# Kernel optimization log

Measured on AMD Instinct MI355X. Metric: run time of the kernel, lower is better.

The kernel has to match this reference:

```python
import jax, jax.numpy as jnp
import numpy as np
from jax import lax

B, T, L = 256, 512, 128


def setup_inputs() -> dict:
    key = jax.random.key(0)
    k1, k2, k3 = jax.random.split(key, 3)
    labels = jax.random.randint(k1, (B, T), 0, L)
    y_true = jax.nn.one_hot(labels, L, dtype=jnp.float32)  # [B,T,L]
    y_pred = jax.random.normal(k2, (B, T, L), dtype=jnp.float32)
    trans = jax.random.normal(k3, (L, L), dtype=jnp.float32) * 0.1
    return {"y_true": y_true, "y_pred": y_pred, "trans": trans}


def reference(y_true, y_pred, trans):
    # ---- log partition via forward algorithm (lax.scan over time) ----
    init = y_pred[:, 0]  # [B,L] initial alpha

    def step(alpha, emit):  # alpha [B,L], emit [B,L]
        # alpha[:, i, None] + trans[i, j] -> logsumexp over previous label i
        new = jax.nn.logsumexp(alpha[:, :, None] + trans[None, :, :], axis=1) + emit
        return new, None

    emits = jnp.swapaxes(y_pred[:, 1:], 0, 1)  # [T-1,B,L]
    final_alpha, _ = lax.scan(step, init, emits)  # [B,L]
    log_norm = jax.nn.logsumexp(final_alpha, axis=1, keepdims=True)  # [B,1]

    # ---- path score (unnormalized log prob of the true path) ----
    point_score = jnp.sum(y_pred * y_true, axis=(1, 2), keepdims=False)[:, None]  # [B,1]
    trans_score = jnp.einsum('bti,btj,ij->b', y_true[:, :-1], y_true[:, 1:], trans)[:, None]  # [B,1]

    return log_norm - (point_score + trans_score)  # [B,1]
```

## Files before the change

### kernel.cpp

```cpp
#include <hip/hip_runtime.h>

typedef float    f32x4  __attribute__((ext_vector_type(4)));
typedef short    s16x8  __attribute__((ext_vector_type(8)));
typedef unsigned uivec2 __attribute__((ext_vector_type(2)));
typedef unsigned uivec4 __attribute__((ext_vector_type(4)));

#define Tt 512
#define Ll 128
#define CH 32
#define CL 16
#define NR 31
#define NRECB 248
#define NSCORE 256

#define WS_PT 0
#define WS_TR 256
#define WS_KR 512
#define WS_KB (512 + 256*NR)
#define WS_RV (512 + 2*256*NR)
#define WS_BV (WS_RV + 256*NR*128)

__device__ __forceinline__ ushort bf16rn(float f) {
  unsigned u = __float_as_uint(f);
  u += 0x7FFFu + ((u >> 16) & 1u);
  return (ushort)(u >> 16);
}
__device__ __forceinline__ unsigned cvtpk(float a, float b) {
  unsigned d;
  asm("v_cvt_pk_bf16_f32 %0, %1, %2" : "=v"(d) : "v"(a), "v"(b));
  return d;
}
__device__ __forceinline__ float4 expf4(float4 v) {
  float4 r; r.x = __expf(v.x); r.y = __expf(v.y); r.z = __expf(v.z); r.w = __expf(v.w);
  return r;
}
__device__ __forceinline__ float4 mul4(float4 v, float s) {
  v.x *= s; v.y *= s; v.z *= s; v.w *= s; return v;
}

__global__ __attribute__((amdgpu_flat_work_group_size(256, 256),
                          amdgpu_waves_per_eu(1)))
void crf_main(const float* __restrict__ yt_g, const float* __restrict__ yp_g,
              const float* __restrict__ tr_g, float* __restrict__ wsf)
{
  __shared__ __align__(16) char smem[32768];
  const int tid = threadIdx.x, wv = tid >> 6, l = tid & 63;
  const int bid = blockIdx.x;

  bool isrec; int sidx = 0, ridx = 0;
  if (bid < 2 * NRECB) { isrec = (bid & 1); sidx = ridx = bid >> 1; }
  else { isrec = false; sidx = NRECB + (bid - 2 * NRECB); }

  if (!isrec) {
    int*   lab_s = (int*)smem;
    float* redp  = (float*)(smem + 2048);
    float* redt  = (float*)(smem + 2080);
    const int b = sidx;
    const float4* yp4 = (const float4*)(yp_g + (size_t)b * Tt * Ll);
    const float4* yt4 = (const float4*)(yt_g + (size_t)b * Tt * Ll);
    float pt = 0.f;
    #pragma unroll 4
    for (int i = 0; i < 64; ++i) {
      int f = tid + i * 256;
      float4 a = yp4[f], y = yt4[f];
      pt += a.x * y.x + a.y * y.y + a.z * y.z + a.w * y.w;
      int t = f >> 5, jb = (f & 31) << 2;
      if (y.x > .5f) lab_s[t] = jb;
      if (y.y > .5f) lab_s[t] = jb + 1;
      if (y.z > .5f) lab_s[t] = jb + 2;
      if (y.w > .5f) lab_s[t] = jb + 3;
    }
    __syncthreads();
    float trl = 0.f;
    for (int t0 = tid; t0 < Tt - 1; t0 += 256)
      trl += tr_g[lab_s[t0] * Ll + lab_s[t0 + 1]];
    #pragma unroll
    for (int o = 32; o; o >>= 1) { pt += __shfl_xor(pt, o); trl += __shfl_xor(trl, o); }
    if (l == 0) { redp[wv] = pt; redt[wv] = trl; }
    __syncthreads();
    if (tid == 0) {
      wsf[WS_PT + b] = redp[0] + redp[1] + redp[2] + redp[3];
      wsf[WS_TR + b] = redt[0] + redt[1] + redt[2] + redt[3];
    }
    return;
  }

  const int task = ridx * 4 + wv;
  const bool FWD = task < 496;
  int g, c;
  if (FWD) { g = task / 31; c = task % 31; }
  else     { int t2 = task - 496; g = t2 / 31; c = t2 % 31 + 1; }
  const int b0  = g * 16;
  const int l15 = l & 15, q = l >> 4;
  const int t_hi = (c == CH - 1) ? (Tt - 1) : (c * CL + CL);
  const int t_lo = c * CL + 1;
  const int n    = FWD ? CL : (t_hi - t_lo + 1);

  s16x8 Bf[8][4];
  if (FWD) {
    #pragma unroll
    for (int kt = 0; kt < 4; ++kt)
      #pragma unroll
      for (int e = 0; e < 8; ++e) {
        const int jin = 32 * kt + 16 * (e >> 2) + 4 * q + (e & 3);
        const float* rp_ = tr_g + jin * Ll + l15;
        #pragma unroll
        for (int tl = 0; tl < 8; ++tl)
          Bf[tl][kt][e] = (short)bf16rn(__expf(rp_[16 * tl]));
      }
  } else {
    #pragma unroll
    for (int tl = 0; tl < 8; ++tl) {
      const float* rp_ = tr_g + (l15 + 16 * tl) * Ll + 4 * q;
      #pragma unroll
      for (int kt = 0; kt < 4; ++kt)
        #pragma unroll
        for (int r = 0; r < 2; ++r) {
          float4 tv = *(const float4*)(rp_ + 32 * kt + 16 * r);
          Bf[tl][kt][4 * r + 0] = (short)bf16rn(__expf(tv.x));
          Bf[tl][kt][4 * r + 1] = (short)bf16rn(__expf(tv.y));
          Bf[tl][kt][4 * r + 2] = (short)bf16rn(__expf(tv.z));
          Bf[tl][kt][4 * r + 3] = (short)bf16rn(__expf(tv.w));
        }
    }
  }

  const unsigned sbase = (unsigned)(size_t)(&smem[0]);
  const unsigned wvoff = (unsigned)(wv * 8192);
  const unsigned lane8 = (unsigned)(l * 8);
  const int wroff = wv * 8192 + l15 * 32 + q * 8;
  const float* emb = yp_g + (size_t)(b0 + l15) * (Tt * Ll) + 4 * q;
  float Kacc = 0.f;

#define LOADSLOT(S, TAU)                                                      \
  { const float* ep_ = emb + (size_t)(TAU) * Ll;                              \
    S##0 = *(const float4*)(ep_ + 0);   S##1 = *(const float4*)(ep_ + 16);    \
    S##2 = *(const float4*)(ep_ + 32);  S##3 = *(const float4*)(ep_ + 48);    \
    S##4 = *(const float4*)(ep_ + 64);  S##5 = *(const float4*)(ep_ + 80);    \
    S##6 = *(const float4*)(ep_ + 96);  S##7 = *(const float4*)(ep_ + 112); }

#define TRREAD8(RBUF, T0,T1,T2,T3,T4,T5,T6,T7)                                \
  { unsigned ra_ = sbase + wvoff + (unsigned)((RBUF) * 4096) + lane8;         \
    asm volatile(                                                             \
      "ds_read_b64_tr_b16 %0, %8 offset:0\n\t"                                \
      "ds_read_b64_tr_b16 %1, %8 offset:512\n\t"                              \
      "ds_read_b64_tr_b16 %2, %8 offset:1024\n\t"                             \
      "ds_read_b64_tr_b16 %3, %8 offset:1536\n\t"                             \
      "ds_read_b64_tr_b16 %4, %8 offset:2048\n\t"                             \
      "ds_read_b64_tr_b16 %5, %8 offset:2560\n\t"                             \
      "ds_read_b64_tr_b16 %6, %8 offset:3072\n\t"                             \
      "ds_read_b64_tr_b16 %7, %8 offset:3584\n\t"                             \
      "s_waitcnt lgkmcnt(0)"                                                  \
      : "=v"(T0), "=v"(T1), "=v"(T2), "=v"(T3),                               \
        "=v"(T4), "=v"(T5), "=v"(T6), "=v"(T7)                                \
      : "v"(ra_) : "memory"); }

#define BUILDA(A_, TA, TB, WA, WB_)                                           \
  { uivec4 au_;                                                               \
    au_.x = cvtpk(__uint_as_float(TA.x << 16) * WA.x,                         \
                  __uint_as_float(TA.x & 0xFFFF0000u) * WA.y);                \
    au_.y = cvtpk(__uint_as_float(TA.y << 16) * WA.z,                         \
                  __uint_as_float(TA.y & 0xFFFF0000u) * WA.w);                \
    au_.z = cvtpk(__uint_as_float(TB.x << 16) * WB_.x,                        \
                  __uint_as_float(TB.x & 0xFFFF0000u) * WB_.y);               \
    au_.w = cvtpk(__uint_as_float(TB.y << 16) * WB_.z,                        \
                  __uint_as_float(TB.y & 0xFFFF0000u) * WB_.w);               \
    A_ = __builtin_bit_cast(s16x8, au_); }

#define MFMAW(WBUF)                                                           \
  { f32x4 dd[8];                                                              \
    _Pragma("unroll")                                                         \
    for (int tl = 0; tl < 8; ++tl) {                                          \
      f32x4 z = {0.f, 0.f, 0.f, 0.f};                                         \
      z = __builtin_amdgcn_mfma_f32_16x16x32_bf16(A0, Bf[tl][0], z, 0, 0, 0); \
      z = __builtin_amdgcn_mfma_f32_16x16x32_bf16(A1, Bf[tl][1], z, 0, 0, 0); \
      z = __builtin_amdgcn_mfma_f32_16x16x32_bf16(A2, Bf[tl][2], z, 0, 0, 0); \
      z = __builtin_amdgcn_mfma_f32_16x16x32_bf16(A3, Bf[tl][3], z, 0, 0, 0); \
      dd[tl] = z;                                                             \
    }                                                                         \
    _Pragma("unroll")                                                         \
    for (int tl = 0; tl < 8; ++tl) {                                          \
      uivec2 w_;                                                              \
      w_.x = cvtpk(dd[tl][0], dd[tl][1]);                                     \
      w_.y = cvtpk(dd[tl][2], dd[tl][3]);                                     \
      *(uivec2*)(smem + wroff + (WBUF) * 4096 + tl * 512) = w_;               \
    } }

#define MULT(RBUF, WBUF, S, REN, PT, PSLOT)                                   \
  { asm volatile("s_waitcnt lgkmcnt(0)" ::: "memory");                        \
    uivec2 t0, t1, t2, t3, t4, t5, t6, t7;                                    \
    TRREAD8(RBUF, t0, t1, t2, t3, t4, t5, t6, t7)                             \
    float4 we0 = expf4(S##0), we1 = expf4(S##1), we2 = expf4(S##2),           \
           we3 = expf4(S##3), we4 = expf4(S##4), we5 = expf4(S##5),           \
           we6 = expf4(S##6), we7 = expf4(S##7);                              \
    if (REN) {                                                                \
      float pf = __uint_as_float(__builtin_amdgcn_readfirstlane(t0.x << 16)); \
      Kacc += __logf(pf);                                                     \
      float rs = __builtin_amdgcn_rcpf(pf);                                   \
      we0 = mul4(we0, rs); we1 = mul4(we1, rs); we2 = mul4(we2, rs);          \
      we3 = mul4(we3, rs); we4 = mul4(we4, rs); we5 = mul4(we5, rs);          \
      we6 = mul4(we6, rs); we7 = mul4(we7, rs);                               \
    }                                                                         \
    s16x8 A0, A1, A2, A3;                                                     \
    BUILDA(A0, t0, t1, we0, we1)                                              \
    BUILDA(A1, t2, t3, we2, we3)                                              \
    BUILDA(A2, t4, t5, we4, we5)                                              \
    BUILDA(A3, t6, t7, we6, we7)                                              \
    MFMAW(WBUF)                                                               \
    if ((PT) >= 0) LOADSLOT(PSLOT, PT) }

  float4 SA0, SA1, SA2, SA3, SA4, SA5, SA6, SA7;
  float4 SB0, SB1, SB2, SB3, SB4, SB5, SB6, SB7;
  const int tau1 = FWD ? (t_lo - 1) : t_hi;
  const int tau2 = FWD ? t_lo : (t_hi - 1);
  LOADSLOT(SB, tau1)
  LOADSLOT(SA, tau2)

  {
    s16x8 A0, A1, A2, A3;
    if (FWD && c > 0) {
      uivec4 au; au.x = au.y = au.z = au.w = 0x3F803F80u;
      A0 = __builtin_bit_cast(s16x8, au); A1 = A0; A2 = A0; A3 = A0;
    } else {
      float4 we0 = expf4(SB0), we1 = expf4(SB1), we2 = expf4(SB2),
             we3 = expf4(SB3), we4 = expf4(SB4), we5 = expf4(SB5),
             we6 = expf4(SB6), we7 = expf4(SB7);
      uivec4 a0; a0.x = cvtpk(we0.x, we0.y); a0.y = cvtpk(we0.z, we0.w);
      a0.z = cvtpk(we1.x, we1.y); a0.w = cvtpk(we1.z, we1.w);
      uivec4 a1; a1.x = cvtpk(we2.x, we2.y); a1.y = cvtpk(we2.z, we2.w);
      a1.z = cvtpk(we3.x, we3.y); a1.w = cvtpk(we3.z, we3.w);
      uivec4 a2; a2.x = cvtpk(we4.x, we4.y); a2.y = cvtpk(we4.z, we4.w);
      a2.z = cvtpk(we5.x, we5.y); a2.w = cvtpk(we5.z, we5.w);
      uivec4 a3; a3.x = cvtpk(we6.x, we6.y); a3.y = cvtpk(we6.z, we6.w);
      a3.z = cvtpk(we7.x, we7.y); a3.w = cvtpk(we7.z, we7.w);
      A0 = __builtin_bit_cast(s16x8, a0); A1 = __builtin_bit_cast(s16x8, a1);
      A2 = __builtin_bit_cast(s16x8, a2); A3 = __builtin_bit_cast(s16x8, a3);
    }
    MFMAW(1)
    const int tau3 = FWD ? (t_lo + 1) : (t_hi - 2);
    LOADSLOT(SB, tau3)
  }

  for (int k = 2; k + 1 <= n; k += 2) {
    const int ta = FWD ? (t_lo + k) : (t_hi - k - 1);
    MULT(1, 0, SA, false, ta, SA)
    const bool ren = ((k + 1) == 9) || ((k + 1) == 15);
    const int tb = (k + 3 <= n + 1) ? (FWD ? (t_lo + k + 1) : (t_hi - k - 2))
                                    : -1;
    MULT(0, 1, SB, ren, tb, SB)
  }
  if ((n & 1) == 0) {
    MULT(1, 0, SA, false, -1, SA)
  }

  {
    asm volatile("s_waitcnt lgkmcnt(0)" ::: "memory");
    uivec2 t0, t1, t2, t3, t4, t5, t6, t7;
    TRREAD8((n & 1), t0, t1, t2, t3, t4, t5, t6, t7)
    float4 wf0, wf1, wf2, wf3, wf4, wf5, wf6, wf7;
    if (FWD) {
      wf0 = expf4(SB0); wf1 = expf4(SB1); wf2 = expf4(SB2); wf3 = expf4(SB3);
      wf4 = expf4(SB4); wf5 = expf4(SB5); wf6 = expf4(SB6); wf7 = expf4(SB7);
    } else {
      float4 one = {1.f, 1.f, 1.f, 1.f};
      wf0 = wf1 = wf2 = wf3 = wf4 = wf5 = wf6 = wf7 = one;
    }
    const int cs = FWD ? c : (c - 1);
    float* rp0 = wsf + (FWD ? WS_RV : WS_BV)
               + ((size_t)(b0 + l15) * NR + cs) * 128 + 4 * q;
#define STOREV(I, T_, W_)                                                     \
    { float4 o_;                                                              \
      o_.x = __uint_as_float(T_.x << 16) * W_.x;                              \
      o_.y = __uint_as_float(T_.x & 0xFFFF0000u) * W_.y;                      \
      o_.z = __uint_as_float(T_.y << 16) * W_.z;                              \
      o_.w = __uint_as_float(T_.y & 0xFFFF0000u) * W_.w;                      \
      *(float4*)(rp0 + 16 * (I)) = o_; }
    STOREV(0, t0, wf0) STOREV(1, t1, wf1) STOREV(2, t2, wf2) STOREV(3, t3, wf3)
    STOREV(4, t4, wf4) STOREV(5, t5, wf5) STOREV(6, t6, wf6) STOREV(7, t7, wf7)
#undef STOREV
    if (q == 0) {
      float* kp = wsf + (FWD ? WS_KR : WS_KB);
      kp[(b0 + l15) * NR + cs] = Kacc;
    }
  }
#undef MULT
#undef MFMAW
#undef BUILDA
#undef TRREAD8
#undef LOADSLOT
}

__global__ __launch_bounds__(64) void crf_stitch(
    const float* __restrict__ wsf, float* __restrict__ out)
{
  const int b = blockIdx.x, j = threadIdx.x;
  const float* RV = wsf + WS_RV + (size_t)b * NR * 128;
  const float* BV = wsf + WS_BV + (size_t)b * NR * 128;
  const float* Kr = wsf + WS_KR + b * NR;
  const float* Kb = wsf + WS_KB + b * NR;
  float lz;
  {
    float d = RV[j] * BV[j] + RV[j + 64] * BV[j + 64];
    #pragma unroll
    for (int o = 32; o; o >>= 1) d += __shfl_xor(d, o);
    lz = __logf(d) + Kr[0] + Kb[0];
  }
  #pragma unroll
  for (int cc = 1; cc < NR; ++cc) {
    float d = RV[cc*128 + j] * BV[cc*128 + j] + RV[cc*128 + j + 64] * BV[cc*128 + j + 64];
    float s = RV[cc*128 + j] + RV[cc*128 + j + 64];
    #pragma unroll
    for (int o = 32; o; o >>= 1) { d += __shfl_xor(d, o); s += __shfl_xor(s, o); }
    lz += __logf(d) - __logf(s) + Kb[cc];
  }
  if (j == 0) out[b] = lz - wsf[WS_PT + b] - wsf[WS_TR + b];
}

extern "C" void kernel_launch(void* const* d_in, const int* in_sizes, int n_in,
                              void* d_out, int out_size, void* d_ws, size_t ws_size,
                              hipStream_t stream) {
  const float* y_true = (const float*)d_in[0];
  const float* y_pred = (const float*)d_in[1];
  const float* trans  = (const float*)d_in[2];
  float* out = (float*)d_out;
  float* wsf = (float*)d_ws;
  crf_main<<<dim3(2 * NRECB + (NSCORE - NRECB)), dim3(256), 0, stream>>>(
      y_true, y_pred, trans, wsf);
  crf_stitch<<<dim3(256), dim3(64), 0, stream>>>(wsf, out);
}
```

Before: 70.92 us.

## Split score computation into separate finer-grained kernel; move transition gather to stitch

The fused kernel that interleaved recurrence blocks with per-batch score blocks is split into three kernels: a recurrence-only kernel, a score kernel that spreads each batch over 8 segment blocks (2048 blocks total) and writes byte labels to the workspace, and the stitch kernel, which now gathers the transition scores and sums the partial point scores. The aim is to give the bandwidth-bound score pass more parallelism and to stop 256-thread score blocks from sharing the grid with the recurrence blocks. The cost is an extra launch, serialisation of the score pass after the recurrence instead of overlapping with it, and extra label traffic through global memory.

```diff
diff --git a/kernel.cpp b/kernel.cpp
--- a/kernel.cpp
+++ b/kernel.cpp
@@ -11,14 +11,14 @@
 #define CL 16
 #define NR 31
 #define NRECB 248
-#define NSCORE 256
-
-#define WS_PT 0
-#define WS_TR 256
-#define WS_KR 512
-#define WS_KB (512 + 256*NR)
-#define WS_RV (512 + 2*256*NR)
-#define WS_BV (WS_RV + 256*NR*128)
+
+#define WS_PTP 0
+#define WS_KR  2048
+#define WS_KB  (2048 + 256*NR)
+#define WS_RV  (2048 + 2*256*NR)
+#define WS_BV  (WS_RV + 256*NR*128)
+#define WS_END (WS_BV + 256*NR*128)
+#define WS_LAB_BYTES ((size_t)WS_END * 4)
 
 __device__ __forceinline__ ushort bf16rn(float f) {
   unsigned u = __float_as_uint(f);
@@ -40,52 +40,13 @@
 
 __global__ __attribute__((amdgpu_flat_work_group_size(256, 256),
                           amdgpu_waves_per_eu(1)))
-void crf_main(const float* __restrict__ yt_g, const float* __restrict__ yp_g,
-              const float* __restrict__ tr_g, float* __restrict__ wsf)
+void crf_rec(const float* __restrict__ yp_g, const float* __restrict__ tr_g,
+             float* __restrict__ wsf)
 {
   __shared__ __align__(16) char smem[32768];
   const int tid = threadIdx.x, wv = tid >> 6, l = tid & 63;
-  const int bid = blockIdx.x;
-
-  bool isrec; int sidx = 0, ridx = 0;
-  if (bid < 2 * NRECB) { isrec = (bid & 1); sidx = ridx = bid >> 1; }
-  else { isrec = false; sidx = NRECB + (bid - 2 * NRECB); }
-
-  if (!isrec) {
-    int*   lab_s = (int*)smem;
-    float* redp  = (float*)(smem + 2048);
-    float* redt  = (float*)(smem + 2080);
-    const int b = sidx;
-    const float4* yp4 = (const float4*)(yp_g + (size_t)b * Tt * Ll);
-    const float4* yt4 = (const float4*)(yt_g + (size_t)b * Tt * Ll);
-    float pt = 0.f;
-    #pragma unroll 4
-    for (int i = 0; i < 64; ++i) {
-      int f = tid + i * 256;
-      float4 a = yp4[f], y = yt4[f];
-      pt += a.x * y.x + a.y * y.y + a.z * y.z + a.w * y.w;
-      int t = f >> 5, jb = (f & 31) << 2;
-      if (y.x > .5f) lab_s[t] = jb;
-      if (y.y > .5f) lab_s[t] = jb + 1;
-      if (y.z > .5f) lab_s[t] = jb + 2;
-      if (y.w > .5f) lab_s[t] = jb + 3;
-    }
-    __syncthreads();
-    float trl = 0.f;
-    for (int t0 = tid; t0 < Tt - 1; t0 += 256)
-      trl += tr_g[lab_s[t0] * Ll + lab_s[t0 + 1]];
-    #pragma unroll
-    for (int o = 32; o; o >>= 1) { pt += __shfl_xor(pt, o); trl += __shfl_xor(trl, o); }
-    if (l == 0) { redp[wv] = pt; redt[wv] = trl; }
-    __syncthreads();
-    if (tid == 0) {
-      wsf[WS_PT + b] = redp[0] + redp[1] + redp[2] + redp[3];
-      wsf[WS_TR + b] = redt[0] + redt[1] + redt[2] + redt[3];
-    }
-    return;
-  }
-
-  const int task = ridx * 4 + wv;
+
+  const int task = blockIdx.x * 4 + wv;
   const bool FWD = task < 496;
   int g, c;
   if (FWD) { g = task / 31; c = task % 31; }
@@ -290,8 +251,39 @@
 #undef LOADSLOT
 }
 
+__global__ __launch_bounds__(256) void crf_score(
+    const float* __restrict__ yt_g, const float* __restrict__ yp_g,
+    float* __restrict__ wsf, unsigned char* __restrict__ lab_g)
+{
+  __shared__ float red[4];
+  const int bid = blockIdx.x;
+  const int b = bid >> 3, seg = bid & 7;
+  const int tid = threadIdx.x, wv = tid >> 6, l = tid & 63;
+  const float4* yp4 = (const float4*)(yp_g + ((size_t)b * Tt + seg * 64) * Ll);
+  const float4* yt4 = (const float4*)(yt_g + ((size_t)b * Tt + seg * 64) * Ll);
+  unsigned char* lb = lab_g + b * Tt + seg * 64;
+  float pt = 0.f;
+  #pragma unroll
+  for (int i = 0; i < 8; ++i) {
+    int f = tid + i * 256;
+    float4 a = yp4[f], y = yt4[f];
+    pt += a.x * y.x + a.y * y.y + a.z * y.z + a.w * y.w;
+    int t = f >> 5, jb = (f & 31) << 2;
+    if (y.x > .5f) lb[t] = (unsigned char)jb;
+    if (y.y > .5f) lb[t] = (unsigned char)(jb + 1);
+    if (y.z > .5f) lb[t] = (unsigned char)(jb + 2);
+    if (y.w > .5f) lb[t] = (unsigned char)(jb + 3);
+  }
+  #pragma unroll
+  for (int o = 32; o; o >>= 1) pt += __shfl_xor(pt, o);
+  if (l == 0) red[wv] = pt;
+  __syncthreads();
+  if (tid == 0) wsf[WS_PTP + b * 8 + seg] = red[0] + red[1] + red[2] + red[3];
+}
+
 __global__ __launch_bounds__(64) void crf_stitch(
-    const float* __restrict__ wsf, float* __restrict__ out)
+    const float* __restrict__ wsf, const unsigned char* __restrict__ lab_g,
+    const float* __restrict__ tr_g, float* __restrict__ out)
 {
   const int b = blockIdx.x, j = threadIdx.x;
   const float* RV = wsf + WS_RV + (size_t)b * NR * 128;
@@ -313,7 +305,16 @@
     for (int o = 32; o; o >>= 1) { d += __shfl_xor(d, o); s += __shfl_xor(s, o); }
     lz += __logf(d) - __logf(s) + Kb[cc];
   }
-  if (j == 0) out[b] = lz - wsf[WS_PT + b] - wsf[WS_TR + b];
+  const unsigned char* lb = lab_g + b * Tt;
+  float tp = (j < 8) ? wsf[WS_PTP + b * 8 + j] : 0.f;
+  #pragma unroll
+  for (int i = 0; i < 8; ++i) {
+    int t = j + i * 64;
+    if (t < Tt - 1) tp += tr_g[(int)lb[t] * Ll + (int)lb[t + 1]];
+  }
+  #pragma unroll
+  for (int o = 32; o; o >>= 1) tp += __shfl_xor(tp, o);
+  if (j == 0) out[b] = lz - tp;
 }
 
 extern "C" void kernel_launch(void* const* d_in, const int* in_sizes, int n_in,
@@ -324,7 +325,8 @@
   const float* trans  = (const float*)d_in[2];
   float* out = (float*)d_out;
   float* wsf = (float*)d_ws;
-  crf_main<<<dim3(2 * NRECB + (NSCORE - NRECB)), dim3(256), 0, stream>>>(
-      y_true, y_pred, trans, wsf);
-  crf_stitch<<<dim3(256), dim3(64), 0, stream>>>(wsf, out);
-}
+  unsigned char* lab = (unsigned char*)d_ws + WS_LAB_BYTES;
+  crf_rec  <<<dim3(NRECB), dim3(256), 0, stream>>>(y_pred, trans, wsf);
+  crf_score<<<dim3(2048),  dim3(256), 0, stream>>>(y_true, y_pred, wsf, lab);
+  crf_stitch<<<dim3(256),  dim3(64),  0, stream>>>(wsf, lab, trans, out);
+}
```

New measurement: 66.96 us. 5.6% less time.
